# Kernel optimization log

Hardware: AMD Instinct MI355X
Metric: run time of the kernel (lower is better)

The kernel has to match this reference:

```python
import jax, jax.numpy as jnp
import numpy as np

B, H, S, D = 4, 16, 2048, 128

def setup_inputs() -> dict:
    key = jax.random.key(0)
    kq, kk, kv = jax.random.split(key, 3)
    query = jax.random.normal(kq, (B, H, S, D), dtype=jnp.float32)
    key_t = jax.random.normal(kk, (B, H, S, D), dtype=jnp.float32)
    value = jax.random.normal(kv, (B, H, S, D), dtype=jnp.float32)
    # causal mask, broadcastable over batch/heads; mask==0 positions are masked out
    mask = jnp.tril(jnp.ones((S, S), dtype=bool))[None, None, :, :]
    return {"query": query, "key": key_t, "value": value, "mask": mask}

def reference(query, key, value, mask):
    d_k = query.shape[-1]
    scale = 1.0 / jnp.sqrt(jnp.asarray(d_k, dtype=query.dtype))
    # [B,H,S,S] attention scores
    scores = jnp.einsum("bhqd,bhkd->bhqk", query, key) * scale
    neg_inf = jnp.asarray(-jnp.inf, dtype=scores.dtype)
    scores = jnp.where(mask, scores, neg_inf)
    weights = jax.nn.softmax(scores, axis=-1)
    return jnp.einsum("bhqk,bhkd->bhqd", weights, value)
```

## Files before the change

### kernel.cpp

```cpp
#include <hip/hip_runtime.h>
#include <hip/hip_bf16.h>
#include <cstdint>

typedef short bf16x8 __attribute__((ext_vector_type(8)));
typedef short bf16x4 __attribute__((ext_vector_type(4)));
typedef float f32x4  __attribute__((ext_vector_type(4)));
typedef float f32x16 __attribute__((ext_vector_type(16)));

#define NB 4
#define NH 16
#define NS 2048
#define ND 128

constexpr int QBLK  = 256;
constexpr int KVBLK = 64;
constexpr int KSZ   = KVBLK * ND;
constexpr int VSZ   = 8 * 1040;


__device__ __forceinline__ unsigned short f2bf(float x) {
  union { __hip_bfloat16 h; unsigned short u; } cv;
  cv.h = __float2bfloat16(x);
  return cv.u;
}

__device__ __forceinline__ bf16x8 pack8(float4 a, float4 b) {
  bf16x8 t;
  t[0] = (short)f2bf(a.x); t[1] = (short)f2bf(a.y);
  t[2] = (short)f2bf(a.z); t[3] = (short)f2bf(a.w);
  t[4] = (short)f2bf(b.x); t[5] = (short)f2bf(b.y);
  t[6] = (short)f2bf(b.z); t[7] = (short)f2bf(b.w);
  return t;
}

__device__ __forceinline__ uint32_t pkbf(float lo, float hi) {
  uint32_t r;
  asm("v_cvt_pk_bf16_f32 %0, %1, %2" : "=v"(r) : "v"(lo), "v"(hi));
  return r;
}

__global__ void __launch_bounds__(512, 2)
attn_fwd(const float* __restrict__ Q, const float* __restrict__ K,
         const float* __restrict__ V, float* __restrict__ Out)
{
  __shared__ __align__(16) unsigned short Ks[2][KSZ];
  __shared__ __align__(16) unsigned short Vs[2][VSZ];
  __shared__ float xS[8][32];

  const int tid = threadIdx.x;
  const int w   = tid >> 6;
  const int l   = tid & 63;
  const int lq  = l & 31;
  const int h   = l >> 5;
  const int lr  = l & 15;
  const int g   = l >> 4;

  const int wgid   = blockIdx.x;
  const int bh     = wgid & 63;
  const int idx    = (wgid >> 6) & 3;
  const int qblock = (wgid < 256) ? (7 - idx) : (idx + 0) + 0*4;
  const int qb     = (wgid < 256) ? (7 - idx) : idx;
  (void)qblock;
  const int qb0    = qb * QBLK;
  const int qw     = qb0 + w * 32;
  const int qrow   = qw + lq;

  const float* Qb = Q + (size_t)bh * NS * ND;
  const float* Kb = K + (size_t)bh * NS * ND;
  const float* Vb = V + (size_t)bh * NS * ND;
  float*       Ob = Out + (size_t)bh * NS * ND;

  const float qscale = 0.08838834764831844f * 1.44269504088896340736f;

  bf16x8 qf[8];
#pragma unroll
  for (int dsl = 0; dsl < 8; ++dsl) {
    const float* src = Qb + (size_t)qrow * ND + dsl * 16 + h * 8;
    float4 a = *(const float4*)src;
    float4 b = *(const float4*)(src + 4);
    a.x *= qscale; a.y *= qscale; a.z *= qscale; a.w *= qscale;
    b.x *= qscale; b.y *= qscale; b.z *= qscale; b.w *= qscale;
    qf[dsl] = pack8(a, b);
  }

  f32x16 of[4];
#pragma unroll
  for (int db = 0; db < 4; ++db)
#pragma unroll
    for (int e = 0; e < 16; ++e) of[db][e] = 0.f;
  float mrow = -1e30f, lsum = 0.f;

  const int srow  = tid >> 3;
  const int c8    = tid & 7;
  const int kofs0 = srow * 256 + ((c8 * 32 +  0) ^ ((srow & 7) << 4));
  const int kofs1 = srow * 256 + ((c8 * 32 + 16) ^ ((srow & 7) << 4));
  const int vofs  = c8 * 1040 + (srow >> 2) * 64 + (srow & 3) * 16;
  const int kswz  = (lq & 7) << 4;

  const int nkv = (qb0 + QBLK) / KVBLK;

  {
    const float* kp = Kb + (size_t)srow * ND + c8 * 16;
    const float* vp = Vb + (size_t)srow * ND + c8 * 16;
    float4 k0 = *(const float4*)(kp + 0), k1 = *(const float4*)(kp + 4);
    float4 k2 = *(const float4*)(kp + 8), k3 = *(const float4*)(kp + 12);
    float4 v0 = *(const float4*)(vp + 0), v1 = *(const float4*)(vp + 4);
    float4 v2 = *(const float4*)(vp + 8), v3 = *(const float4*)(vp + 12);
    *(bf16x8*)((char*)&Ks[0][0] + kofs0) = pack8(k0, k1);
    *(bf16x8*)((char*)&Ks[0][0] + kofs1) = pack8(k2, k3);
    *(bf16x8*)&Vs[0][vofs]     = pack8(v0, v1);
    *(bf16x8*)&Vs[0][vofs + 8] = pack8(v2, v3);
  }
  __syncthreads();

  int cur = 0;
  for (int it = 0; it < nkv; ++it) {
    const int kbase = it * KVBLK;
    const bool pre = (it + 1 < nkv);

    float4 kr0, kr1, kr2, kr3, vr0, vr1, vr2, vr3;
    if (pre) {
      const float* kp = Kb + (size_t)(kbase + KVBLK + srow) * ND + c8 * 16;
      const float* vp = Vb + (size_t)(kbase + KVBLK + srow) * ND + c8 * 16;
      kr0 = *(const float4*)(kp + 0); kr1 = *(const float4*)(kp + 4);
      kr2 = *(const float4*)(kp + 8); kr3 = *(const float4*)(kp + 12);
      vr0 = *(const float4*)(vp + 0); vr1 = *(const float4*)(vp + 4);
      vr2 = *(const float4*)(vp + 8); vr3 = *(const float4*)(vp + 12);
    }

    if (kbase <= qw + 31) {
      const char* ksb = (const char*)&Ks[cur][0];
      f32x16 st[2];
#pragma unroll
      for (int e = 0; e < 16; ++e) { st[0][e] = 0.f; st[1][e] = 0.f; }
#pragma unroll
      for (int sub = 0; sub < 2; ++sub)
#pragma unroll
        for (int dsl = 0; dsl < 8; ++dsl) {
          bf16x8 kf = *(const bf16x8*)(ksb + (sub * 32 + lq) * 256 +
                                       ((dsl * 32 + h * 16) ^ kswz));
          st[sub] = __builtin_amdgcn_mfma_f32_32x32x16_bf16(kf, qf[dsl], st[sub], 0, 0, 0);
        }

      if (kbase + 63 > qw) {
        const int thr = qrow - kbase - 4 * h;
#pragma unroll
        for (int sub = 0; sub < 2; ++sub)
#pragma unroll
          for (int r = 0; r < 16; ++r) {
            const int kls = sub * 32 + (r & 3) + 8 * (r >> 2);
            st[sub][r] = (kls > thr) ? -1e30f : st[sub][r];
          }
      }

      float t8[8];
#pragma unroll
      for (int i = 0; i < 8; ++i) t8[i] = fmaxf(st[0][i], st[0][i + 8]);
#pragma unroll
      for (int i = 0; i < 8; ++i) t8[i] = fmaxf(t8[i], fmaxf(st[1][i], st[1][i + 8]));
      float vm = fmaxf(fmaxf(fmaxf(t8[0], t8[1]), fmaxf(t8[2], t8[3])),
                       fmaxf(fmaxf(t8[4], t8[5]), fmaxf(t8[6], t8[7])));
      vm = fmaxf(vm, __shfl_xor(vm, 32));

      const bool defer = __all(vm <= mrow + 8.f);
      if (!defer) {
        const float mnew  = fmaxf(mrow, vm);
        const float alpha = exp2f(mrow - mnew);
        mrow = mnew;
        lsum *= alpha;
        xS[w][lq] = alpha;
        asm volatile("s_waitcnt lgkmcnt(0)" ::: "memory");
        f32x4 a4[4];
#pragma unroll
        for (int t = 0; t < 4; ++t) a4[t] = *(const f32x4*)&xS[w][t * 8 + 4 * h];
#pragma unroll
        for (int db = 0; db < 4; ++db)
#pragma unroll
          for (int r = 0; r < 16; ++r) of[db][r] *= a4[r >> 2][r & 3];
      }

#pragma unroll
      for (int sub = 0; sub < 2; ++sub)
#pragma unroll
        for (int r = 0; r < 16; ++r)
          st[sub][r] = exp2f(st[sub][r] - mrow);
      float s8[8];
#pragma unroll
      for (int i = 0; i < 8; ++i) s8[i] = st[0][i] + st[0][i + 8];
#pragma unroll
      for (int i = 0; i < 8; ++i) s8[i] += st[1][i] + st[1][i + 8];
      float ps = ((s8[0] + s8[1]) + (s8[2] + s8[3])) +
                 ((s8[4] + s8[5]) + (s8[6] + s8[7]));
      ps += __shfl_xor(ps, 32);
      lsum += ps;

      bf16x8 pa[4];
#pragma unroll
      for (int sub = 0; sub < 2; ++sub) {
        uint32_t c0 = pkbf(st[sub][0],  st[sub][1]);
        uint32_t c1 = pkbf(st[sub][2],  st[sub][3]);
        uint32_t c2 = pkbf(st[sub][4],  st[sub][5]);
        uint32_t c3 = pkbf(st[sub][6],  st[sub][7]);
        uint32_t c4 = pkbf(st[sub][8],  st[sub][9]);
        uint32_t c5 = pkbf(st[sub][10], st[sub][11]);
        uint32_t c6 = pkbf(st[sub][12], st[sub][13]);
        uint32_t c7 = pkbf(st[sub][14], st[sub][15]);
        asm volatile("v_permlane32_swap_b32 %0, %1" : "+v"(c0), "+v"(c2));
        asm volatile("v_permlane32_swap_b32 %0, %1" : "+v"(c1), "+v"(c3));
        asm volatile("v_permlane32_swap_b32 %0, %1" : "+v"(c4), "+v"(c6));
        asm volatile("v_permlane32_swap_b32 %0, %1" : "+v"(c5), "+v"(c7));
        union { uint32_t u[4]; bf16x8 v; } f0, f1;
        f0.u[0] = c0; f0.u[1] = c1; f0.u[2] = c2; f0.u[3] = c3;
        f1.u[0] = c4; f1.u[1] = c5; f1.u[2] = c6; f1.u[3] = c7;
        pa[sub * 2 + 0] = f0.v;
        pa[sub * 2 + 1] = f1.v;
      }

      asm volatile("s_waitcnt lgkmcnt(0)" ::: "memory");
      const uint32_t vb = (uint32_t)(uintptr_t)&Vs[cur][0] +
                          (uint32_t)((g & 1) * 2080 + (g >> 1) * 256 + lr * 8);
      bf16x4 ta0, ta1, tb0, tb1;

#define TR2(P0, P1, DB, S)                                                     \
      asm volatile("ds_read_b64_tr_b16 %0, %2 offset:%c3\n\t"                  \
                   "ds_read_b64_tr_b16 %1, %2 offset:%c4"                      \
                   : "=v"(P0), "=v"(P1)                                        \
                   : "v"(vb), "i"((DB)*4160 + (S)*512), "i"((DB)*4160 + (S)*512 + 128));

#define PVS(DB, S, PX0, PX1, WAITN)                                            \
      asm volatile("s_waitcnt lgkmcnt(" #WAITN ")" ::: "memory");              \
      __builtin_amdgcn_sched_barrier(0);                                       \
      { union { struct { bf16x4 lo, hi; } p; bf16x8 v; } uu;                   \
        uu.p.lo = PX0; uu.p.hi = PX1;                                          \
        of[DB] = __builtin_amdgcn_mfma_f32_32x32x16_bf16(pa[S], uu.v, of[DB], 0, 0, 0); }

      TR2(ta0, ta1, 0, 0);
      TR2(tb0, tb1, 1, 0);
      __builtin_amdgcn_s_setprio(1);
      PVS(0, 0, ta0, ta1, 2); TR2(ta0, ta1, 2, 0);
      PVS(1, 0, tb0, tb1, 2); TR2(tb0, tb1, 3, 0);
      PVS(2, 0, ta0, ta1, 2); TR2(ta0, ta1, 0, 1);
      PVS(3, 0, tb0, tb1, 2); TR2(tb0, tb1, 1, 1);
      PVS(0, 1, ta0, ta1, 2); TR2(ta0, ta1, 2, 1);
      PVS(1, 1, tb0, tb1, 2); TR2(tb0, tb1, 3, 1);
      PVS(2, 1, ta0, ta1, 2); TR2(ta0, ta1, 0, 2);
      PVS(3, 1, tb0, tb1, 2); TR2(tb0, tb1, 1, 2);
      PVS(0, 2, ta0, ta1, 2); TR2(ta0, ta1, 2, 2);
      PVS(1, 2, tb0, tb1, 2); TR2(tb0, tb1, 3, 2);
      PVS(2, 2, ta0, ta1, 2); TR2(ta0, ta1, 0, 3);
      PVS(3, 2, tb0, tb1, 2); TR2(tb0, tb1, 1, 3);
      PVS(0, 3, ta0, ta1, 2); TR2(ta0, ta1, 2, 3);
      PVS(1, 3, tb0, tb1, 2); TR2(tb0, tb1, 3, 3);
      PVS(2, 3, ta0, ta1, 2);
      PVS(3, 3, tb0, tb1, 0);
      __builtin_amdgcn_s_setprio(0);
#undef TR2
#undef PVS
    }

    if (pre) {
      const int nxt = cur ^ 1;
      *(bf16x8*)((char*)&Ks[nxt][0] + kofs0) = pack8(kr0, kr1);
      *(bf16x8*)((char*)&Ks[nxt][0] + kofs1) = pack8(kr2, kr3);
      *(bf16x8*)&Vs[nxt][vofs]     = pack8(vr0, vr1);
      *(bf16x8*)&Vs[nxt][vofs + 8] = pack8(vr2, vr3);
    }
    __syncthreads();
    cur ^= 1;
  }

  xS[w][lq] = 1.0f / lsum;
  asm volatile("s_waitcnt lgkmcnt(0)" ::: "memory");
  f32x4 inv4[4];
#pragma unroll
  for (int t = 0; t < 4; ++t) inv4[t] = *(const f32x4*)&xS[w][t * 8 + 4 * h];
#pragma unroll
  for (int t = 0; t < 4; ++t)
#pragma unroll
    for (int j = 0; j < 4; ++j) {
      const int qr = qw + t * 8 + 4 * h + j;
      const float iv = inv4[t][j];
#pragma unroll
      for (int db = 0; db < 4; ++db)
        Ob[(size_t)qr * ND + db * 32 + lq] = of[db][t * 4 + j] * iv;
    }
}

extern "C" void kernel_launch(void* const* d_in, const int* in_sizes, int n_in,
                              void* d_out, int out_size, void* d_ws, size_t ws_size,
                              hipStream_t stream) {
  const float* Q = (const float*)d_in[0];
  const float* K = (const float*)d_in[1];
  const float* V = (const float*)d_in[2];
  float* O = (float*)d_out;

  attn_fwd<<<dim3((NS / QBLK) * NB * NH), dim3(512), 0, stream>>>(Q, K, V, O);
}
```

Baseline: 296.2 us.

## Halve query tile, single-buffer K/V in LDS, raise occupancy with balanced scheduling

Shrinks the query block from 256 to 128 rows (4 waves per block instead of 8) and drops LDS double buffering, so each block now loads the next K/V tile synchronously between two barriers. Launch bounds change to 256 threads with 3 blocks per CU, and the block-to-query-tile mapping is reordered so heavy and light causal tiles interleave. The aim is more resident blocks and better load balance across the doubled grid. The cost is that global loads are no longer overlapped with compute inside a block, and there is an extra barrier per iteration.

```diff
diff --git a/kernel.cpp b/kernel.cpp
--- a/kernel.cpp
+++ b/kernel.cpp
@@ -12,7 +12,7 @@
 #define NS 2048
 #define ND 128
 
-constexpr int QBLK  = 256;
+constexpr int QBLK  = 128;
 constexpr int KVBLK = 64;
 constexpr int KSZ   = KVBLK * ND;
 constexpr int VSZ   = 8 * 1040;
@@ -39,13 +39,13 @@
   return r;
 }
 
-__global__ void __launch_bounds__(512, 2)
+__global__ void __launch_bounds__(256, 3)
 attn_fwd(const float* __restrict__ Q, const float* __restrict__ K,
          const float* __restrict__ V, float* __restrict__ Out)
 {
-  __shared__ __align__(16) unsigned short Ks[2][KSZ];
-  __shared__ __align__(16) unsigned short Vs[2][VSZ];
-  __shared__ float xS[8][32];
+  __shared__ __align__(16) unsigned short Ks[KSZ];
+  __shared__ __align__(16) unsigned short Vs[VSZ];
+  __shared__ float xS[4][32];
 
   const int tid = threadIdx.x;
   const int w   = tid >> 6;
@@ -55,15 +55,17 @@
   const int lr  = l & 15;
   const int g   = l >> 4;
 
-  const int wgid   = blockIdx.x;
-  const int bh     = wgid & 63;
-  const int idx    = (wgid >> 6) & 3;
-  const int qblock = (wgid < 256) ? (7 - idx) : (idx + 0) + 0*4;
-  const int qb     = (wgid < 256) ? (7 - idx) : idx;
-  (void)qblock;
-  const int qb0    = qb * QBLK;
-  const int qw     = qb0 + w * 32;
-  const int qrow   = qw + lq;
+  const int wgid = blockIdx.x;
+  const int bh   = wgid & 63;
+  const int sidx = wgid >> 6;
+  const int s2   = sidx & 3, sc = sidx >> 2;
+  const int qb   = (sc == 0) ? (15 - 2 * s2)
+                 : (sc == 1) ? (2 * s2)
+                 : (sc == 2) ? (14 - 2 * s2)
+                 :             (1 + 2 * s2);
+  const int qb0  = qb * QBLK;
+  const int qw   = qb0 + w * 32;
+  const int qrow = qw + lq;
 
   const float* Qb = Q + (size_t)bh * NS * ND;
   const float* Kb = K + (size_t)bh * NS * ND;
@@ -90,46 +92,49 @@
     for (int e = 0; e < 16; ++e) of[db][e] = 0.f;
   float mrow = -1e30f, lsum = 0.f;
 
-  const int srow  = tid >> 3;
-  const int c8    = tid & 7;
-  const int kofs0 = srow * 256 + ((c8 * 32 +  0) ^ ((srow & 7) << 4));
-  const int kofs1 = srow * 256 + ((c8 * 32 + 16) ^ ((srow & 7) << 4));
-  const int vofs  = c8 * 1040 + (srow >> 2) * 64 + (srow & 3) * 16;
-  const int kswz  = (lq & 7) << 4;
-
-  const int nkv = (qb0 + QBLK) / KVBLK;
-
-  {
-    const float* kp = Kb + (size_t)srow * ND + c8 * 16;
-    const float* vp = Vb + (size_t)srow * ND + c8 * 16;
-    float4 k0 = *(const float4*)(kp + 0), k1 = *(const float4*)(kp + 4);
-    float4 k2 = *(const float4*)(kp + 8), k3 = *(const float4*)(kp + 12);
-    float4 v0 = *(const float4*)(vp + 0), v1 = *(const float4*)(vp + 4);
-    float4 v2 = *(const float4*)(vp + 8), v3 = *(const float4*)(vp + 12);
-    *(bf16x8*)((char*)&Ks[0][0] + kofs0) = pack8(k0, k1);
-    *(bf16x8*)((char*)&Ks[0][0] + kofs1) = pack8(k2, k3);
-    *(bf16x8*)&Vs[0][vofs]     = pack8(v0, v1);
-    *(bf16x8*)&Vs[0][vofs + 8] = pack8(v2, v3);
+  const int srow = tid >> 2;
+  const int fc   = (tid & 3) * 32;
+  const int swz  = (srow & 7) << 4;
+  int kofs[4], vofs[4];
+#pragma unroll
+  for (int cc = 0; cc < 4; ++cc) {
+    kofs[cc] = srow * 256 + ((2 * fc + 16 * cc) ^ swz);
+    vofs[cc] = ((fc + 8 * cc) >> 4) * 1040 + (srow >> 2) * 64 +
+               (srow & 3) * 16 + ((8 * cc) & 8);
   }
+  const int kswz = (lq & 7) << 4;
+
+  const int nkv = 2 * qb + 2;
+
+#define STAGE(KB)                                                           \
+  {                                                                         \
+    const float* kp = Kb + (size_t)((KB) + srow) * ND + fc;                 \
+    const float* vp = Vb + (size_t)((KB) + srow) * ND + fc;                 \
+    float4 q0 = *(const float4*)(kp + 0),  q1 = *(const float4*)(kp + 4);   \
+    float4 q2 = *(const float4*)(kp + 8),  q3 = *(const float4*)(kp + 12);  \
+    float4 q4 = *(const float4*)(kp + 16), q5 = *(const float4*)(kp + 20);  \
+    float4 q6 = *(const float4*)(kp + 24), q7 = *(const float4*)(kp + 28);  \
+    *(bf16x8*)((char*)&Ks[0] + kofs[0]) = pack8(q0, q1);                    \
+    *(bf16x8*)((char*)&Ks[0] + kofs[1]) = pack8(q2, q3);                    \
+    *(bf16x8*)((char*)&Ks[0] + kofs[2]) = pack8(q4, q5);                    \
+    *(bf16x8*)((char*)&Ks[0] + kofs[3]) = pack8(q6, q7);                    \
+    q0 = *(const float4*)(vp + 0);  q1 = *(const float4*)(vp + 4);          \
+    q2 = *(const float4*)(vp + 8);  q3 = *(const float4*)(vp + 12);         \
+    q4 = *(const float4*)(vp + 16); q5 = *(const float4*)(vp + 20);         \
+    q6 = *(const float4*)(vp + 24); q7 = *(const float4*)(vp + 28);         \
+    *(bf16x8*)&Vs[vofs[0]] = pack8(q0, q1);                                 \
+    *(bf16x8*)&Vs[vofs[1]] = pack8(q2, q3);                                 \
+    *(bf16x8*)&Vs[vofs[2]] = pack8(q4, q5);                                 \
+    *(bf16x8*)&Vs[vofs[3]] = pack8(q6, q7);                                 \
+  }
+
+  STAGE(0);
   __syncthreads();
 
-  int cur = 0;
   for (int it = 0; it < nkv; ++it) {
     const int kbase = it * KVBLK;
-    const bool pre = (it + 1 < nkv);
-
-    float4 kr0, kr1, kr2, kr3, vr0, vr1, vr2, vr3;
-    if (pre) {
-      const float* kp = Kb + (size_t)(kbase + KVBLK + srow) * ND + c8 * 16;
-      const float* vp = Vb + (size_t)(kbase + KVBLK + srow) * ND + c8 * 16;
-      kr0 = *(const float4*)(kp + 0); kr1 = *(const float4*)(kp + 4);
-      kr2 = *(const float4*)(kp + 8); kr3 = *(const float4*)(kp + 12);
-      vr0 = *(const float4*)(vp + 0); vr1 = *(const float4*)(vp + 4);
-      vr2 = *(const float4*)(vp + 8); vr3 = *(const float4*)(vp + 12);
-    }
 
     if (kbase <= qw + 31) {
-      const char* ksb = (const char*)&Ks[cur][0];
       f32x16 st[2];
 #pragma unroll
       for (int e = 0; e < 16; ++e) { st[0][e] = 0.f; st[1][e] = 0.f; }
@@ -137,7 +142,8 @@
       for (int sub = 0; sub < 2; ++sub)
 #pragma unroll
         for (int dsl = 0; dsl < 8; ++dsl) {
-          bf16x8 kf = *(const bf16x8*)(ksb + (sub * 32 + lq) * 256 +
+          bf16x8 kf = *(const bf16x8*)((const char*)&Ks[0] +
+                                       (sub * 32 + lq) * 256 +
                                        ((dsl * 32 + h * 16) ^ kswz));
           st[sub] = __builtin_amdgcn_mfma_f32_32x32x16_bf16(kf, qf[dsl], st[sub], 0, 0, 0);
         }
@@ -217,7 +223,7 @@
       }
 
       asm volatile("s_waitcnt lgkmcnt(0)" ::: "memory");
-      const uint32_t vb = (uint32_t)(uintptr_t)&Vs[cur][0] +
+      const uint32_t vb = (uint32_t)(uintptr_t)&Vs[0] +
                           (uint32_t)((g & 1) * 2080 + (g >> 1) * 256 + lr * 8);
       bf16x4 ta0, ta1, tb0, tb1;
 
@@ -258,16 +264,13 @@
 #undef PVS
     }
 
-    if (pre) {
-      const int nxt = cur ^ 1;
-      *(bf16x8*)((char*)&Ks[nxt][0] + kofs0) = pack8(kr0, kr1);
-      *(bf16x8*)((char*)&Ks[nxt][0] + kofs1) = pack8(kr2, kr3);
-      *(bf16x8*)&Vs[nxt][vofs]     = pack8(vr0, vr1);
-      *(bf16x8*)&Vs[nxt][vofs + 8] = pack8(vr2, vr3);
+    __syncthreads();
+    if (it + 1 < nkv) {
+      STAGE(kbase + KVBLK);
     }
     __syncthreads();
-    cur ^= 1;
   }
+#undef STAGE
 
   xS[w][lq] = 1.0f / lsum;
   asm volatile("s_waitcnt lgkmcnt(0)" ::: "memory");
@@ -294,5 +297,5 @@
   const float* V = (const float*)d_in[2];
   float* O = (float*)d_out;
 
-  attn_fwd<<<dim3((NS / QBLK) * NB * NH), dim3(512), 0, stream>>>(Q, K, V, O);
-}
+  attn_fwd<<<dim3((NS / QBLK) * NB * NH), dim3(256), 0, stream>>>(Q, K, V, O);
+}
```

Result: slower. 445.3 us (+50.3%).
